# Kernel optimization log

Measured on AMD Instinct MI355X. Metric: run time of the kernel, lower is better.

## Reference

```python
import jax, jax.numpy as jnp
import numpy as np

B, N, T, D = 8, 32, 49, 4
K = 4            # edge_types
HE = 256         # encoder_hidden
HD = 256         # decoder_hidden (msg_hid == msg_out == n_hid)
TEMP = 0.5
SKIP_FIRST = True
EPS = 1e-5
E = N * (N - 1)  # 992 directed edges (off-diagonal)


def setup_inputs() -> dict:
    key = jax.random.key(0)
    ks = jax.random.split(key, 32)
    it = iter(range(32))

    def lin(fi, fo):
        k = ks[next(it)]
        return (jax.random.normal(k, (fi, fo), jnp.float32) / np.sqrt(fi)).astype(jnp.float32)

    def bias(fo):
        return jnp.full((fo,), 0.1, jnp.float32)

    off = ~np.eye(N, dtype=bool)
    recv_np, send_np = np.where(off)  # rel_rec rows, rel_send cols
    recv_idx = jnp.asarray(recv_np, jnp.int32)
    send_idx = jnp.asarray(send_np, jnp.int32)

    data = jax.random.normal(ks[next(it)], (B, N, T, D), jnp.float32)
    u = jax.random.uniform(ks[next(it)], (B, E, K), jnp.float32, 1e-6, 1.0 - 1e-6)
    gumbel = -jnp.log(-jnp.log(u))

    inp = {"data": data, "gumbel": gumbel, "recv_idx": recv_idx, "send_idx": send_idx}
    # Encoder: 4 MLPs (fc1, fc2, bn gamma/beta) + fc_out
    enc_dims = [(T * D, HE), (2 * HE, HE), (HE, HE), (3 * HE, HE)]
    for i, (fi, fh) in enumerate(enc_dims, start=1):
        inp[f"e{i}_w1"] = lin(fi, HE)
        inp[f"e{i}_b1"] = bias(HE)
        inp[f"e{i}_w2"] = lin(HE, HE)
        inp[f"e{i}_b2"] = bias(HE)
        inp[f"e{i}_g"] = jnp.ones((HE,), jnp.float32)
        inp[f"e{i}_be"] = jnp.zeros((HE,), jnp.float32)
    inp["fc_w"] = lin(HE, K)
    inp["fc_b"] = bias(K)
    # Decoder: per-edge-type message MLPs (stacked) + output MLP
    inp["mw1"] = jnp.stack([lin(2 * D, HD) for _ in range(K)])
    inp["mb1"] = jnp.zeros((K, HD), jnp.float32)
    inp["mw2"] = jnp.stack([lin(HD, HD) for _ in range(K)])
    inp["mb2"] = jnp.zeros((K, HD), jnp.float32)
    inp["ow1"] = lin(D + HD, HD)
    inp["ob1"] = jnp.zeros((HD,), jnp.float32)
    inp["ow2"] = lin(HD, HD)
    inp["ob2"] = jnp.zeros((HD,), jnp.float32)
    inp["ow3"] = lin(HD, D)
    inp["ob3"] = jnp.zeros((D,), jnp.float32)
    return inp


def _mlp(x, w1, b1, w2, b2, g, be):
    # Two-layer ELU net + batch norm over all leading dims (training-mode stats).
    x = jax.nn.elu(x @ w1 + b1)
    x = jax.nn.elu(x @ w2 + b2)
    m = x.mean(axis=(0, 1), keepdims=True)
    v = x.var(axis=(0, 1), keepdims=True)
    return (x - m) / jnp.sqrt(v + EPS) * g + be


def reference(data, gumbel, recv_idx, send_idx,
              e1_w1, e1_b1, e1_w2, e1_b2, e1_g, e1_be,
              e2_w1, e2_b1, e2_w2, e2_b2, e2_g, e2_be,
              e3_w1, e3_b1, e3_w2, e3_b2, e3_g, e3_be,
              e4_w1, e4_b1, e4_w2, e4_b2, e4_g, e4_be,
              fc_w, fc_b, mw1, mb1, mw2, mb2,
              ow1, ob1, ow2, ob2, ow3, ob3):
    # ---------- Encoder ----------
    x = data.reshape(B, N, T * D)
    x = _mlp(x, e1_w1, e1_b1, e1_w2, e1_b2, e1_g, e1_be)          # [B,N,HE]
    edges = jnp.concatenate([x[:, send_idx], x[:, recv_idx]], -1)  # [B,E,2HE]
    x = _mlp(edges, e2_w1, e2_b1, e2_w2, e2_b2, e2_g, e2_be)       # [B,E,HE]
    x_skip = x
    # edge2node: rel_rec^T @ x == scatter-add by receiver, then /N
    incoming = jnp.zeros((B, N, HE), x.dtype).at[:, recv_idx, :].add(x) / N
    x = _mlp(incoming, e3_w1, e3_b1, e3_w2, e3_b2, e3_g, e3_be)    # [B,N,HE]
    edges2 = jnp.concatenate([x[:, send_idx], x[:, recv_idx]], -1)  # [B,E,2HE]
    x = jnp.concatenate([edges2, x_skip], -1)                       # [B,E,3HE]
    x = _mlp(x, e4_w1, e4_b1, e4_w2, e4_b2, e4_g, e4_be)
    logits = x @ fc_w + fc_b                                        # [B,E,K]

    rel_type = jax.nn.softmax((logits + gumbel) / TEMP, axis=-1)    # gumbel-softmax (soft)
    prob = jax.nn.softmax(logits, axis=-1)

    # ---------- Decoder (pred_steps=1) ----------
    inputs = jnp.transpose(data, (0, 2, 1, 3))                      # [B,T,N,D]
    rt = rel_type[:, None, :, :]                                    # [B,1,E,K] broadcast over T
    senders = inputs[:, :, send_idx, :]                             # [B,T,E,D]
    receivers = inputs[:, :, recv_idx, :]
    pre_msg = jnp.concatenate([senders, receivers], -1)             # [B,T,E,2D]

    start = 1 if SKIP_FIRST else 0
    all_msgs = jnp.zeros((B, T, E, HD), pre_msg.dtype)
    for k in range(start, K):
        msg = jax.nn.relu(pre_msg @ mw1[k] + mb1[k])
        msg = jax.nn.relu(msg @ mw2[k] + mb2[k])
        all_msgs = all_msgs + msg * rt[..., k:k + 1]

    # scatter-sum messages to receiving nodes
    agg = jnp.zeros((B, T, N, HD), all_msgs.dtype).at[:, :, recv_idx, :].add(all_msgs)
    aug = jnp.concatenate([inputs, agg], -1)                        # [B,T,N,D+HD]
    p = jax.nn.relu(aug @ ow1 + ob1)
    p = jax.nn.relu(p @ ow2 + ob2)
    p = p @ ow3 + ob3
    step = inputs + p                                               # [B,T,N,D]

    output = jnp.transpose(step[:, :T - 1], (0, 2, 1, 3))           # [B,N,T-1,D]
    return (output, prob)
```

## Files before the change

kernel.cpp:

```cpp
#include <hip/hip_runtime.h>
#include <hip/hip_bf16.h>

#define NNODES 32
#define TSTEPS 49
#define NEDGE  992
#define ROWS_E 7936
#define ROWS_OUT 12544
#define EPSV 1e-5f

typedef __hip_bfloat16 bf16;
typedef __attribute__((ext_vector_type(8))) short bf16x8;
typedef __attribute__((ext_vector_type(4))) float f32x4;

__device__ inline float eluf(float x){ return x > 0.f ? x : (__expf(x) - 1.f); }
__device__ inline float bfu2f(unsigned short u){ unsigned v = ((unsigned)u) << 16; return *reinterpret_cast<float*>(&v); }
__device__ inline unsigned pack_bf16(float a, float b){
  __hip_bfloat16 ha = __float2bfloat16(a), hb = __float2bfloat16(b);
  unsigned short ua = *reinterpret_cast<unsigned short*>(&ha);
  unsigned short ub = *reinterpret_cast<unsigned short*>(&hb);
  return (unsigned)ua | ((unsigned)ub << 16);
}

__global__ void prep_weights(const float* e2w1, const float* e2w2, const float* e4w1, const float* e4w2,
                             const float* mw2, const float* ow1, const float* ow2,
                             const float* e2b1, const float* e4b1,
                             bf16* w2abT, bf16* w2bT, bf16* w4abT, bf16* w4cT, bf16* w4bT,
                             bf16* mw2T, bf16* ow1T, bf16* ow2T,
                             float* bias2, float* bias4, float* zerob){
  int i = blockIdx.x*256 + threadIdx.x;
  if (i < 131072){ int n=i>>8, c=i&255;
    w2abT[i] = __float2bfloat16(n<256 ? e2w1[c*256+n] : e2w1[(256+c)*256 + (n-256)]); return;} i-=131072;
  if (i < 65536){ int n=i>>8,c=i&255; w2bT[i]=__float2bfloat16(e2w2[c*256+n]); return;} i-=65536;
  if (i < 131072){ int n=i>>8,c=i&255;
    w4abT[i]=__float2bfloat16(n<256 ? e4w1[c*256+n] : e4w1[(256+c)*256+(n-256)]); return;} i-=131072;
  if (i < 65536){ int n=i>>8,c=i&255; w4cT[i]=__float2bfloat16(e4w1[(512+c)*256+n]); return;} i-=65536;
  if (i < 65536){ int n=i>>8,c=i&255; w4bT[i]=__float2bfloat16(e4w2[c*256+n]); return;} i-=65536;
  if (i < 262144){ int k=i>>16, r=i&65535; int n=r>>8,c=r&255;
    mw2T[i]=__float2bfloat16(mw2[(k*256+c)*256+n]); return;} i-=262144;
  if (i < 73728){ int n=i/288, c=i%288;
    ow1T[i]= (c<260)?__float2bfloat16(ow1[c*256+n]):__float2bfloat16(0.f); return;} i-=73728;
  if (i < 65536){ int n=i>>8,c=i&255; ow2T[i]=__float2bfloat16(ow2[c*256+n]); return;} i-=65536;
  if (i < 512){ bias2[i] = (i<256)?e2b1[i]:0.f; return;} i-=512;
  if (i < 512){ bias4[i] = (i<256)?e4b1[i]:0.f; return;} i-=512;
  if (i < 256){ zerob[i]=0.f; return; }
}

template<int KIN>
__global__ void small_mlp(const float* __restrict__ X, const float* __restrict__ w1, const float* __restrict__ b1,
                          const float* __restrict__ w2, const float* __restrict__ b2, float* __restrict__ H){
  __shared__ float xs[KIN];
  __shared__ float h1[256];
  int r = blockIdx.x, f = threadIdx.x;
  for (int c = f; c < KIN; c += 256) xs[c] = X[(size_t)r*KIN + c];
  __syncthreads();
  float acc = b1[f];
  for (int c = 0; c < KIN; c++) acc = fmaf(xs[c], w1[c*256+f], acc);
  h1[f] = eluf(acc);
  __syncthreads();
  float a2 = b2[f];
  for (int c = 0; c < 256; c++) a2 = fmaf(h1[c], w2[c*256+f], a2);
  H[(size_t)r*256 + f] = eluf(a2);
}

__global__ void bn_small(const float* __restrict__ H, const float* __restrict__ g, const float* __restrict__ be,
                         bf16* __restrict__ Xout){
  int f = threadIdx.x;
  float s = 0.f, s2 = 0.f;
  for (int r = 0; r < 256; r++){ float v = H[r*256+f]; s += v; s2 += v*v; }
  float m = s * (1.f/256.f), var = s2 * (1.f/256.f) - m*m;
  float sc = g[f] * rsqrtf(var + EPSV), sh = be[f] - m*sc;
  for (int r = 0; r < 256; r++) Xout[r*256+f] = __float2bfloat16(H[r*256+f]*sc + sh);
}

template<int K, int NCOLS, int ACT, bool OBF, int MT, bool STATS>
__global__ __launch_bounds__(256,4) void gemm_mfma(const bf16* __restrict__ A, const bf16* __restrict__ WT,
                                                   const float* __restrict__ bias, void* __restrict__ Y,
                                                   float* __restrict__ part){
  constexpr int NTW = NCOLS/64;
  int mb = blockIdx.x;
  int tid = threadIdx.x;
  int w = tid >> 6, l = tid & 63, l15 = l & 15, lq = l >> 4;
  f32x4 acc[MT/16][NTW];
  #pragma unroll
  for (int m = 0; m < MT/16; m++)
    #pragma unroll
    for (int nt = 0; nt < NTW; nt++) acc[m][nt] = (f32x4){0.f,0.f,0.f,0.f};
  const bf16* Ab = A + (size_t)mb*MT*K;
  int nw = w*(NCOLS/4);
  for (int s = 0; s < K/32; s++){
    int c0 = s*32 + lq*8;
    bf16x8 bfr[NTW];
    #pragma unroll
    for (int nt = 0; nt < NTW; nt++){
      int fcol = nw + nt*16 + l15;
      bfr[nt] = *reinterpret_cast<const bf16x8*>(WT + (size_t)fcol*K + c0);
    }
    #pragma unroll
    for (int m = 0; m < MT/16; m++){
      bf16x8 afr = *reinterpret_cast<const bf16x8*>(Ab + (size_t)(m*16 + l15)*K + c0);
      #pragma unroll
      for (int nt = 0; nt < NTW; nt++)
        acc[m][nt] = __builtin_amdgcn_mfma_f32_16x16x32_bf16(afr, bfr[nt], acc[m][nt], 0, 0, 0);
    }
  }
  #pragma unroll
  for (int nt = 0; nt < NTW; nt++){
    int fcol = nw + nt*16 + l15;
    float bv = bias[fcol];
    float cs = 0.f, cs2 = 0.f;
    #pragma unroll
    for (int m = 0; m < MT/16; m++){
      #pragma unroll
      for (int v = 0; v < 4; v++){
        int row = mb*MT + m*16 + lq*4 + v;
        float val = acc[m][nt][v] + bv;
        if (ACT == 1) val = fmaxf(val, 0.f);
        else if (ACT == 2) val = eluf(val);
        if (OBF) ((bf16*)Y)[(size_t)row*NCOLS + fcol] = __float2bfloat16(val);
        else     ((float*)Y)[(size_t)row*NCOLS + fcol] = val;
        if (STATS){ cs += val; cs2 += val*val; }
      }
    }
    if (STATS){
      cs  += __shfl_xor(cs, 16);  cs  += __shfl_xor(cs, 32);
      cs2 += __shfl_xor(cs2, 16); cs2 += __shfl_xor(cs2, 32);
      if (l < 16){ part[(size_t)mb*512 + fcol] = cs; part[(size_t)mb*512 + 256 + fcol] = cs2; }
    }
  }
}

__global__ void combine2(const bf16* __restrict__ SR, bf16* __restrict__ Y){
  int i = blockIdx.x*256 + threadIdx.x;
  int row = i >> 5, c8 = (i & 31)*8;
  int b = row / NEDGE, e = row % NEDGE;
  int rc = e / 31, jj = e % 31;
  int sn = jj + (jj >= rc);
  bf16x8 s8 = *reinterpret_cast<const bf16x8*>(SR + (size_t)(b*NNODES + sn)*512 + c8);
  bf16x8 r8 = *reinterpret_cast<const bf16x8*>(SR + (size_t)(b*NNODES + rc)*512 + 256 + c8);
  bf16x8 o;
  #pragma unroll
  for (int k = 0; k < 8; k++){
    float v = bfu2f((unsigned short)s8[k]) + bfu2f((unsigned short)r8[k]);
    v = eluf(v);
    __hip_bfloat16 h = __float2bfloat16(v);
    o[k] = *reinterpret_cast<short*>(&h);
  }
  *reinterpret_cast<bf16x8*>(Y + (size_t)row*256 + c8) = o;
}

__global__ void combine4(const bf16* __restrict__ SR, const float* __restrict__ Z, bf16* __restrict__ Y){
  int i = blockIdx.x*256 + threadIdx.x;
  int row = i >> 5, c8 = (i & 31)*8;
  int b = row / NEDGE, e = row % NEDGE;
  int rc = e / 31, jj = e % 31;
  int sn = jj + (jj >= rc);
  bf16x8 s8 = *reinterpret_cast<const bf16x8*>(SR + (size_t)(b*NNODES + sn)*512 + c8);
  bf16x8 r8 = *reinterpret_cast<const bf16x8*>(SR + (size_t)(b*NNODES + rc)*512 + 256 + c8);
  const float* zp = Z + (size_t)row*256 + c8;
  float4 z0 = *reinterpret_cast<const float4*>(zp);
  float4 z1 = *reinterpret_cast<const float4*>(zp+4);
  float zz[8] = {z0.x,z0.y,z0.z,z0.w,z1.x,z1.y,z1.z,z1.w};
  bf16x8 o;
  #pragma unroll
  for (int k = 0; k < 8; k++){
    float v = bfu2f((unsigned short)s8[k]) + bfu2f((unsigned short)r8[k]) + zz[k];
    v = eluf(v);
    __hip_bfloat16 h = __float2bfloat16(v);
    o[k] = *reinterpret_cast<short*>(&h);
  }
  *reinterpret_cast<bf16x8*>(Y + (size_t)row*256 + c8) = o;
}

__global__ void bn_finalize(const float* __restrict__ part, int nb, const float* __restrict__ g,
                            const float* __restrict__ be, float* __restrict__ prm, float nrows){
  int f = threadIdx.x;
  float s = 0.f, s2 = 0.f;
  for (int i = 0; i < nb; i++){ s += part[(size_t)i*512+f]; s2 += part[(size_t)i*512+256+f]; }
  float m = s / nrows, var = s2 / nrows - m*m;
  float sc = g[f] * rsqrtf(var + EPSV);
  prm[f] = sc; prm[256+f] = be[f] - m*sc;
}
__global__ void bn_apply(const float* __restrict__ Y, const float* __restrict__ prm, bf16* __restrict__ X){
  int i = blockIdx.x*256 + threadIdx.x;
  int c8 = (i & 31)*8;
  const float* yp = Y + (size_t)i*8;
  float4 a0 = *reinterpret_cast<const float4*>(yp);
  float4 a1 = *reinterpret_cast<const float4*>(yp+4);
  float4 s0 = *reinterpret_cast<const float4*>(prm + c8);
  float4 s1 = *reinterpret_cast<const float4*>(prm + c8 + 4);
  float4 h0 = *reinterpret_cast<const float4*>(prm + 256 + c8);
  float4 h1 = *reinterpret_cast<const float4*>(prm + 256 + c8 + 4);
  float vals[8] = {a0.x*s0.x+h0.x, a0.y*s0.y+h0.y, a0.z*s0.z+h0.z, a0.w*s0.w+h0.w,
                   a1.x*s1.x+h1.x, a1.y*s1.y+h1.y, a1.z*s1.z+h1.z, a1.w*s1.w+h1.w};
  bf16x8 o;
  #pragma unroll
  for (int k = 0; k < 8; k++){
    __hip_bfloat16 h = __float2bfloat16(vals[k]);
    o[k] = *reinterpret_cast<short*>(&h);
  }
  *reinterpret_cast<bf16x8*>(X + (size_t)i*8) = o;
}

__global__ void seg_incoming(const bf16* __restrict__ X2, float* __restrict__ inc){
  int bn = blockIdx.x; int b = bn >> 5, n = bn & 31;
  int f = threadIdx.x;
  const bf16* p = X2 + (size_t)(b*NEDGE + n*31)*256 + f;
  float s = 0.f;
  for (int j = 0; j < 31; j++) s += __bfloat162float(p[j*256]);
  inc[bn*256 + f] = s * (1.f/32.f);
}

__global__ void fc_softmax(const bf16* __restrict__ X4, const float* __restrict__ fcw, const float* __restrict__ fcb,
                           const float* __restrict__ gumbel, float* __restrict__ prob_out, float* __restrict__ rt){
  int r = blockIdx.x*256 + threadIdx.x;
  if (r >= ROWS_E) return;
  float l0 = fcb[0], l1 = fcb[1], l2 = fcb[2], l3 = fcb[3];
  const bf16* xr = X4 + (size_t)r*256;
  for (int c = 0; c < 256; c += 8){
    uint4 u = *reinterpret_cast<const uint4*>(xr + c);
    unsigned uu[4] = {u.x, u.y, u.z, u.w};
    #pragma unroll
    for (int q = 0; q < 4; q++){
      float x0 = bfu2f((unsigned short)(uu[q] & 0xffff));
      float x1 = bfu2f((unsigned short)(uu[q] >> 16));
      int cc = c + 2*q;
      float4 w0 = *reinterpret_cast<const float4*>(fcw + cc*4);
      float4 w1 = *reinterpret_cast<const float4*>(fcw + (cc+1)*4);
      l0 += x0*w0.x + x1*w1.x; l1 += x0*w0.y + x1*w1.y;
      l2 += x0*w0.z + x1*w1.z; l3 += x0*w0.w + x1*w1.w;
    }
  }
  float mx = fmaxf(fmaxf(l0,l1), fmaxf(l2,l3));
  float e0 = __expf(l0-mx), e1 = __expf(l1-mx), e2 = __expf(l2-mx), e3 = __expf(l3-mx);
  float inv = 1.f / (e0+e1+e2+e3);
  prob_out[(size_t)r*4+0] = e0*inv; prob_out[(size_t)r*4+1] = e1*inv;
  prob_out[(size_t)r*4+2] = e2*inv; prob_out[(size_t)r*4+3] = e3*inv;
  float4 gv = *reinterpret_cast<const float4*>(gumbel + (size_t)r*4);
  float t0 = (l0+gv.x)*2.f, t1 = (l1+gv.y)*2.f, t2 = (l2+gv.z)*2.f, t3 = (l3+gv.w)*2.f;
  float mx2 = fmaxf(fmaxf(t0,t1), fmaxf(t2,t3));
  float f0 = __expf(t0-mx2), f1 = __expf(t1-mx2), f2 = __expf(t2-mx2), f3 = __expf(t3-mx2);
  float inv2 = 1.f / (f0+f1+f2+f3);
  rt[(size_t)r*4+0] = f0*inv2; rt[(size_t)r*4+1] = f1*inv2;
  rt[(size_t)r*4+2] = f2*inv2; rt[(size_t)r*4+3] = f3*inv2;
}

__global__ __launch_bounds__(256,2) void decoder_msg(
    const float* __restrict__ data, const float* __restrict__ rt,
    const float* __restrict__ mw1, const float* __restrict__ mb1,
    const bf16* __restrict__ mw2T, const float* __restrict__ mb2,
    bf16* __restrict__ Aaug){
  __shared__ __align__(16) short hA[128*256];
  __shared__ __align__(16) float xn[32][4];
  __shared__ __align__(16) float rts_s[128][4];
  __shared__ __align__(16) float aggl[4][256];
  int bx = blockIdx.x;
  int bt = bx >> 3, rg = bx & 7;
  int b = bt / TSTEPS, t = bt % TSTEPS;
  int n0 = rg * 4;
  int tid = threadIdx.x;
  int w = tid >> 6, l = tid & 63, l15 = l & 15, lq = l >> 4;

  if (tid < 32){
    xn[tid][0] = data[((size_t)(b*NNODES + tid)*TSTEPS + t)*4 + 0];
    xn[tid][1] = data[((size_t)(b*NNODES + tid)*TSTEPS + t)*4 + 1];
    xn[tid][2] = data[((size_t)(b*NNODES + tid)*TSTEPS + t)*4 + 2];
    xn[tid][3] = data[((size_t)(b*NNODES + tid)*TSTEPS + t)*4 + 3];
  } else if (tid >= 64 && tid < 192){
    int r = tid - 64;
    int n = n0 + (r >> 5), j = r & 31;
    float4 rv = make_float4(0.f,0.f,0.f,0.f);
    if (j < 31) rv = *reinterpret_cast<const float4*>(rt + ((size_t)(b*NEDGE + n*31 + j))*4);
    *reinterpret_cast<float4*>(&rts_s[r][0]) = rv;
  }
  for (int i = tid; i < 1024; i += 256) ((float*)aggl)[i] = 0.f;
  __syncthreads();

  int p = tid & 127, hf = tid >> 7;
  int rc0 = n0 + 2*hf, rc1 = rc0 + 1;
  int c0b = 4*p;

  for (int kk = 1; kk < 4; kk++){
    {
      float wS0x,wS0y,wS1x,wS1y,wS2x,wS2y,wS3x,wS3y;
      float wR0x,wR0y,wR1x,wR1y,wR2x,wR2y,wR3x,wR3y;
      {
        float2 a0 = *reinterpret_cast<const float2*>(mw1 + (size_t)(kk*8+0)*256 + 2*p);
        float2 a1 = *reinterpret_cast<const float2*>(mw1 + (size_t)(kk*8+1)*256 + 2*p);
        float2 a2 = *reinterpret_cast<const float2*>(mw1 + (size_t)(kk*8+2)*256 + 2*p);
        float2 a3 = *reinterpret_cast<const float2*>(mw1 + (size_t)(kk*8+3)*256 + 2*p);
        float2 a4 = *reinterpret_cast<const float2*>(mw1 + (size_t)(kk*8+4)*256 + 2*p);
        float2 a5 = *reinterpret_cast<const float2*>(mw1 + (size_t)(kk*8+5)*256 + 2*p);
        float2 a6 = *reinterpret_cast<const float2*>(mw1 + (size_t)(kk*8+6)*256 + 2*p);
        float2 a7 = *reinterpret_cast<const float2*>(mw1 + (size_t)(kk*8+7)*256 + 2*p);
        wS0x=a0.x; wS0y=a0.y; wS1x=a1.x; wS1y=a1.y; wS2x=a2.x; wS2y=a2.y; wS3x=a3.x; wS3y=a3.y;
        wR0x=a4.x; wR0y=a4.y; wR1x=a5.x; wR1y=a5.y; wR2x=a6.x; wR2y=a6.y; wR3x=a7.x; wR3y=a7.y;
      }
      float2 bb = *reinterpret_cast<const float2*>(mb1 + kk*256 + 2*p);
      float Sa[32], Sb[32];
      #pragma unroll
      for (int nd = 0; nd < 32; nd++){
        float4 x = *reinterpret_cast<float4*>(&xn[nd][0]);
        Sa[nd] = fmaf(x.x,wS0x, fmaf(x.y,wS1x, fmaf(x.z,wS2x, fmaf(x.w,wS3x, bb.x))));
        Sb[nd] = fmaf(x.x,wS0y, fmaf(x.y,wS1y, fmaf(x.z,wS2y, fmaf(x.w,wS3y, bb.y))));
      }
      float4 x0 = *reinterpret_cast<float4*>(&xn[rc0][0]);
      float4 x1 = *reinterpret_cast<float4*>(&xn[rc1][0]);
      float Ra0 = fmaf(x0.x,wR0x, fmaf(x0.y,wR1x, fmaf(x0.z,wR2x, x0.w*wR3x)));
      float Rb0 = fmaf(x0.x,wR0y, fmaf(x0.y,wR1y, fmaf(x0.z,wR2y, x0.w*wR3y)));
      float Ra1 = fmaf(x1.x,wR0x, fmaf(x1.y,wR1x, fmaf(x1.z,wR2x, x1.w*wR3x)));
      float Rb1 = fmaf(x1.x,wR0y, fmaf(x1.y,wR1y, fmaf(x1.z,wR2y, x1.w*wR3y)));
      char* hAb = reinterpret_cast<char*>(hA);
      #pragma unroll
      for (int jj = 0; jj < 32; jj++){
        {
          int r = hf*64 + jj;
          unsigned pk = 0u;
          if (jj < 31){
            bool sel = (jj >= rc0);
            float sa = sel ? Sa[jj+1] : Sa[jj];
            float sb = sel ? Sb[jj+1] : Sb[jj];
            pk = pack_bf16(fmaxf(sa + Ra0, 0.f), fmaxf(sb + Rb0, 0.f));
          }
          *reinterpret_cast<unsigned*>(hAb + r*512 + (c0b ^ ((r & 7) << 4))) = pk;
        }
        {
          int r = hf*64 + 32 + jj;
          unsigned pk = 0u;
          if (jj < 31){
            bool sel = (jj >= rc1);
            float sa = sel ? Sa[jj+1] : Sa[jj];
            float sb = sel ? Sb[jj+1] : Sb[jj];
            pk = pack_bf16(fmaxf(sa + Ra1, 0.f), fmaxf(sb + Rb1, 0.f));
          }
          *reinterpret_cast<unsigned*>(hAb + r*512 + (c0b ^ ((r & 7) << 4))) = pk;
        }
      }
    }
    __syncthreads();

    f32x4 acc[8][4];
    #pragma unroll
    for (int m = 0; m < 8; m++)
      #pragma unroll
      for (int nt = 0; nt < 4; nt++) acc[m][nt] = (f32x4){0.f,0.f,0.f,0.f};
    const bf16* wk = mw2T + (size_t)kk*65536;
    for (int s = 0; s < 8; s++){
      int c0 = s*32 + lq*8;
      bf16x8 bfr[4];
      #pragma unroll
      for (int nt = 0; nt < 4; nt++){
        int fcol = w*64 + nt*16 + l15;
        bfr[nt] = *reinterpret_cast<const bf16x8*>(wk + (size_t)fcol*256 + c0);
      }
      #pragma unroll
      for (int m = 0; m < 8; m++){
        int rowm = m*16 + l15;
        int byteoff = rowm*512 + ((s*64 + lq*16) ^ ((rowm & 7) << 4));
        bf16x8 af = *reinterpret_cast<const bf16x8*>(reinterpret_cast<const char*>(hA) + byteoff);
        #pragma unroll
        for (int nt = 0; nt < 4; nt++)
          acc[m][nt] = __builtin_amdgcn_mfma_f32_16x16x32_bf16(af, bfr[nt], acc[m][nt], 0, 0, 0);
      }
    }
    #pragma unroll
    for (int m = 0; m < 8; m++){
      int g = m >> 1;
      #pragma unroll
      for (int nt = 0; nt < 4; nt++){
        int fcol = w*64 + nt*16 + l15;
        float bv = mb2[kk*256 + fcol];
        float ssum = 0.f;
        #pragma unroll
        for (int v = 0; v < 4; v++){
          int rowa = m*16 + lq*4 + v;
          float msg = fmaxf(acc[m][nt][v] + bv, 0.f);
          ssum += msg * rts_s[rowa][kk];
        }
        ssum += __shfl_xor(ssum, 16);
        ssum += __shfl_xor(ssum, 32);
        if (lq == 0) aggl[g][fcol] += ssum;
      }
    }
    __syncthreads();
  }

  for (int i = tid; i < 4*288; i += 256){
    int g = i / 288, c = i % 288;
    float val;
    if (c < 4)        val = xn[n0+g][c];
    else if (c < 260) val = aggl[g][c-4];
    else              val = 0.f;
    Aaug[(size_t)(bt*NNODES + n0 + g)*288 + c] = __float2bfloat16(val);
  }
}

__global__ void final_out(const bf16* __restrict__ P2, const float* __restrict__ ow3,
                          const float* __restrict__ ob3, const float* __restrict__ data,
                          float* __restrict__ out){
  int r = blockIdx.x*256 + threadIdx.x;
  if (r >= ROWS_OUT) return;
  int bt = r >> 5, n = r & 31;
  int b = bt / TSTEPS, t = bt % TSTEPS;
  float a0 = ob3[0], a1 = ob3[1], a2 = ob3[2], a3 = ob3[3];
  const bf16* pr = P2 + (size_t)r*256;
  for (int c = 0; c < 256; c += 8){
    uint4 u = *reinterpret_cast<const uint4*>(pr + c);
    unsigned uu[4] = {u.x, u.y, u.z, u.w};
    #pragma unroll
    for (int q = 0; q < 4; q++){
      float x0 = bfu2f((unsigned short)(uu[q] & 0xffff));
      float x1 = bfu2f((unsigned short)(uu[q] >> 16));
      int cc = c + 2*q;
      float4 w0 = *reinterpret_cast<const float4*>(ow3 + cc*4);
      float4 w1 = *reinterpret_cast<const float4*>(ow3 + (cc+1)*4);
      a0 += x0*w0.x + x1*w1.x; a1 += x0*w0.y + x1*w1.y;
      a2 += x0*w0.z + x1*w1.z; a3 += x0*w0.w + x1*w1.w;
    }
  }
  if (t < TSTEPS-1){
    float4 dv = *reinterpret_cast<const float4*>(data + ((size_t)(b*NNODES + n)*TSTEPS + t)*4);
    float4 o; o.x = dv.x + a0; o.y = dv.y + a1; o.z = dv.z + a2; o.w = dv.w + a3;
    *reinterpret_cast<float4*>(out + ((size_t)(b*NNODES + n)*(TSTEPS-1) + t)*4) = o;
  }
}

extern "C" void kernel_launch(void* const* d_in, const int* in_sizes, int n_in,
                              void* d_out, int out_size, void* d_ws, size_t ws_size,
                              hipStream_t stream){
  const float* data    = (const float*)d_in[0];
  const float* gumbel  = (const float*)d_in[1];
  const float* e1_w1=(const float*)d_in[4],  *e1_b1=(const float*)d_in[5],
             * e1_w2=(const float*)d_in[6],  *e1_b2=(const float*)d_in[7],
             * e1_g =(const float*)d_in[8],  *e1_be=(const float*)d_in[9];
  const float* e2_w1=(const float*)d_in[10], *e2_b1=(const float*)d_in[11],
             * e2_w2=(const float*)d_in[12], *e2_b2=(const float*)d_in[13],
             * e2_g =(const float*)d_in[14], *e2_be=(const float*)d_in[15];
  const float* e3_w1=(const float*)d_in[16], *e3_b1=(const float*)d_in[17],
             * e3_w2=(const float*)d_in[18], *e3_b2=(const float*)d_in[19],
             * e3_g =(const float*)d_in[20], *e3_be=(const float*)d_in[21];
  const float* e4_w1=(const float*)d_in[22], *e4_b1=(const float*)d_in[23],
             * e4_w2=(const float*)d_in[24], *e4_b2=(const float*)d_in[25],
             * e4_g =(const float*)d_in[26], *e4_be=(const float*)d_in[27];
  const float* fc_w=(const float*)d_in[28], *fc_b=(const float*)d_in[29];
  const float* mw1=(const float*)d_in[30], *mb1=(const float*)d_in[31];
  const float* mw2=(const float*)d_in[32], *mb2=(const float*)d_in[33];
  const float* ow1=(const float*)d_in[34], *ob1=(const float*)d_in[35];
  const float* ow2=(const float*)d_in[36], *ob2=(const float*)d_in[37];
  const float* ow3=(const float*)d_in[38], *ob3=(const float*)d_in[39];

  char* ws = (char*)d_ws;
  size_t off = 0;
  auto alloc = [&](size_t bytes)->void*{ void* p = ws + off; off = (off + bytes + 255) & ~(size_t)255; return p; };
  bf16* W2ABT= (bf16*)alloc((size_t)131072*2);
  bf16* W2BT = (bf16*)alloc((size_t)65536*2);
  bf16* W4ABT= (bf16*)alloc((size_t)131072*2);
  bf16* W4CT = (bf16*)alloc((size_t)65536*2);
  bf16* W4BT = (bf16*)alloc((size_t)65536*2);
  bf16* MW2T = (bf16*)alloc((size_t)262144*2);
  bf16* OW1T = (bf16*)alloc((size_t)73728*2);
  bf16* OW2T = (bf16*)alloc((size_t)65536*2);
  float* BIAS2=(float*)alloc((size_t)512*4);
  float* BIAS4=(float*)alloc((size_t)512*4);
  float* ZEROB=(float*)alloc((size_t)256*4);
  bf16* X1   = (bf16*)alloc((size_t)65536*2);
  float* HS  = (float*)alloc((size_t)65536*4);
  bf16* X3   = (bf16*)alloc((size_t)65536*2);
  bf16* SR2  = (bf16*)alloc((size_t)131072*2);
  bf16* SR4  = (bf16*)alloc((size_t)131072*2);
  float* Z4  = (float*)alloc((size_t)7936*256*4);
  bf16* YBF  = (bf16*)alloc((size_t)12544*256*2);
  float* YF32= (float*)alloc((size_t)7936*256*4);
  bf16* X2   = (bf16*)alloc((size_t)7936*256*2);
  bf16* X4   = (bf16*)alloc((size_t)7936*256*2);
  bf16* P2   = (bf16*)alloc((size_t)12544*256*2);
  float* INC = (float*)alloc((size_t)65536*4);
  float* RT  = (float*)alloc((size_t)7936*4*4);
  float* PART= (float*)alloc((size_t)248*512*4);
  float* PRM = (float*)alloc((size_t)512*4);
  bf16* AAUG = (bf16*)alloc((size_t)12544*288*2);

  float* out = (float*)d_out;
  float* prob_out = out + 49152;

  prep_weights<<<3365,256,0,stream>>>(e2_w1,e2_w2,e4_w1,e4_w2,mw2,ow1,ow2,e2_b1,e4_b1,
                                      W2ABT,W2BT,W4ABT,W4CT,W4BT,MW2T,OW1T,OW2T,BIAS2,BIAS4,ZEROB);
  small_mlp<196><<<256,256,0,stream>>>(data, e1_w1,e1_b1,e1_w2,e1_b2, HS);
  bn_small<<<1,256,0,stream>>>(HS, e1_g, e1_be, X1);
  gemm_mfma<256,512,0,true,32,false><<<8,256,0,stream>>>(X1, W2ABT, BIAS2, SR2, nullptr);
  combine2<<<992,256,0,stream>>>(SR2, YBF);
  gemm_mfma<256,256,2,false,32,true><<<248,256,0,stream>>>(YBF, W2BT, e2_b2, YF32, PART);
  bn_finalize<<<1,256,0,stream>>>(PART, 248, e2_g, e2_be, PRM, 7936.f);
  bn_apply<<<992,256,0,stream>>>(YF32, PRM, X2);
  seg_incoming<<<256,256,0,stream>>>(X2, INC);
  small_mlp<256><<<256,256,0,stream>>>(INC, e3_w1,e3_b1,e3_w2,e3_b2, HS);
  bn_small<<<1,256,0,stream>>>(HS, e3_g, e3_be, X3);
  gemm_mfma<256,512,0,true,32,false><<<8,256,0,stream>>>(X3, W4ABT, BIAS4, SR4, nullptr);
  gemm_mfma<256,256,0,false,32,false><<<248,256,0,stream>>>(X2, W4CT, ZEROB, Z4, nullptr);
  combine4<<<992,256,0,stream>>>(SR4, Z4, YBF);
  gemm_mfma<256,256,2,false,32,true><<<248,256,0,stream>>>(YBF, W4BT, e4_b2, YF32, PART);
  bn_finalize<<<1,256,0,stream>>>(PART, 248, e4_g, e4_be, PRM, 7936.f);
  bn_apply<<<992,256,0,stream>>>(YF32, PRM, X4);
  fc_softmax<<<31,256,0,stream>>>(X4, fc_w, fc_b, gumbel, prob_out, RT);
  decoder_msg<<<3136,256,0,stream>>>(data, RT, mw1, mb1, MW2T, mb2, AAUG);
  gemm_mfma<288,256,1,true,32,false><<<392,256,0,stream>>>(AAUG, OW1T, ob1, YBF, nullptr);
  gemm_mfma<256,256,1,true,32,false><<<392,256,0,stream>>>(YBF, OW2T, ob2, P2, nullptr);
  final_out<<<49,256,0,stream>>>(P2, ow3, ob3, data, out);
}
```

Before: 626.4 us.

## Halve decoder_msg tile to two receiver nodes per block for higher occupancy

```diff
diff --git a/kernel.cpp b/kernel.cpp
--- a/kernel.cpp
+++ b/kernel.cpp
@@ -14,11 +14,10 @@
 
 __device__ inline float eluf(float x){ return x > 0.f ? x : (__expf(x) - 1.f); }
 __device__ inline float bfu2f(unsigned short u){ unsigned v = ((unsigned)u) << 16; return *reinterpret_cast<float*>(&v); }
-__device__ inline unsigned pack_bf16(float a, float b){
-  __hip_bfloat16 ha = __float2bfloat16(a), hb = __float2bfloat16(b);
-  unsigned short ua = *reinterpret_cast<unsigned short*>(&ha);
-  unsigned short ub = *reinterpret_cast<unsigned short*>(&hb);
-  return (unsigned)ua | ((unsigned)ub << 16);
+__device__ inline unsigned cvt_pk_bf16(float lo, float hi){
+  unsigned r;
+  asm("v_cvt_pk_bf16_f32 %0, %1, %2" : "=v"(r) : "v"(lo), "v"(hi));
+  return r;
 }
 
 __global__ void prep_weights(const float* e2w1, const float* e2w2, const float* e4w1, const float* e4w2,
@@ -244,103 +243,97 @@
   rt[(size_t)r*4+2] = f2*inv2; rt[(size_t)r*4+3] = f3*inv2;
 }
 
-__global__ __launch_bounds__(256,2) void decoder_msg(
+__global__ __launch_bounds__(256,4) void decoder_msg(
     const float* __restrict__ data, const float* __restrict__ rt,
     const float* __restrict__ mw1, const float* __restrict__ mb1,
     const bf16* __restrict__ mw2T, const float* __restrict__ mb2,
     bf16* __restrict__ Aaug){
-  __shared__ __align__(16) short hA[128*256];
+  __shared__ __align__(16) short hA[64*256];
   __shared__ __align__(16) float xn[32][4];
-  __shared__ __align__(16) float rts_s[128][4];
-  __shared__ __align__(16) float aggl[4][256];
+  __shared__ __align__(16) float rts_s[64][4];
+  __shared__ __align__(16) float aggl[2][256];
   int bx = blockIdx.x;
-  int bt = bx >> 3, rg = bx & 7;
+  int bt = bx >> 4, rg = bx & 15;
   int b = bt / TSTEPS, t = bt % TSTEPS;
-  int n0 = rg * 4;
+  int n0 = rg * 2;
   int tid = threadIdx.x;
   int w = tid >> 6, l = tid & 63, l15 = l & 15, lq = l >> 4;
 
   if (tid < 32){
-    xn[tid][0] = data[((size_t)(b*NNODES + tid)*TSTEPS + t)*4 + 0];
-    xn[tid][1] = data[((size_t)(b*NNODES + tid)*TSTEPS + t)*4 + 1];
-    xn[tid][2] = data[((size_t)(b*NNODES + tid)*TSTEPS + t)*4 + 2];
-    xn[tid][3] = data[((size_t)(b*NNODES + tid)*TSTEPS + t)*4 + 3];
-  } else if (tid >= 64 && tid < 192){
+    *reinterpret_cast<float4*>(&xn[tid][0]) =
+        *reinterpret_cast<const float4*>(data + ((size_t)(b*NNODES + tid)*TSTEPS + t)*4);
+  } else if (tid >= 64 && tid < 128){
     int r = tid - 64;
     int n = n0 + (r >> 5), j = r & 31;
     float4 rv = make_float4(0.f,0.f,0.f,0.f);
     if (j < 31) rv = *reinterpret_cast<const float4*>(rt + ((size_t)(b*NEDGE + n*31 + j))*4);
     *reinterpret_cast<float4*>(&rts_s[r][0]) = rv;
   }
-  for (int i = tid; i < 1024; i += 256) ((float*)aggl)[i] = 0.f;
+  for (int i = tid; i < 512; i += 256) ((float*)aggl)[i] = 0.f;
+  {
+    unsigned* hw = reinterpret_cast<unsigned*>(hA);
+    hw[(tid < 128) ? (31*128 + tid) : (63*128 + (tid - 128))] = 0u;
+  }
   __syncthreads();
 
-  int p = tid & 127, hf = tid >> 7;
-  int rc0 = n0 + 2*hf, rc1 = rc0 + 1;
-  int c0b = 4*p;
+  int c2 = tid & 127;
+  int rh = tid >> 7;
+  int xorbase = 4*c2;
 
   for (int kk = 1; kk < 4; kk++){
     {
-      float wS0x,wS0y,wS1x,wS1y,wS2x,wS2y,wS3x,wS3y;
-      float wR0x,wR0y,wR1x,wR1y,wR2x,wR2y,wR3x,wR3y;
-      {
-        float2 a0 = *reinterpret_cast<const float2*>(mw1 + (size_t)(kk*8+0)*256 + 2*p);
-        float2 a1 = *reinterpret_cast<const float2*>(mw1 + (size_t)(kk*8+1)*256 + 2*p);
-        float2 a2 = *reinterpret_cast<const float2*>(mw1 + (size_t)(kk*8+2)*256 + 2*p);
-        float2 a3 = *reinterpret_cast<const float2*>(mw1 + (size_t)(kk*8+3)*256 + 2*p);
-        float2 a4 = *reinterpret_cast<const float2*>(mw1 + (size_t)(kk*8+4)*256 + 2*p);
-        float2 a5 = *reinterpret_cast<const float2*>(mw1 + (size_t)(kk*8+5)*256 + 2*p);
-        float2 a6 = *reinterpret_cast<const float2*>(mw1 + (size_t)(kk*8+6)*256 + 2*p);
-        float2 a7 = *reinterpret_cast<const float2*>(mw1 + (size_t)(kk*8+7)*256 + 2*p);
-        wS0x=a0.x; wS0y=a0.y; wS1x=a1.x; wS1y=a1.y; wS2x=a2.x; wS2y=a2.y; wS3x=a3.x; wS3y=a3.y;
-        wR0x=a4.x; wR0y=a4.y; wR1x=a5.x; wR1y=a5.y; wR2x=a6.x; wR2y=a6.y; wR3x=a7.x; wR3y=a7.y;
+      float2 a0 = *reinterpret_cast<const float2*>(mw1 + (size_t)(kk*8+0)*256 + 2*c2);
+      float2 a1 = *reinterpret_cast<const float2*>(mw1 + (size_t)(kk*8+1)*256 + 2*c2);
+      float2 a2 = *reinterpret_cast<const float2*>(mw1 + (size_t)(kk*8+2)*256 + 2*c2);
+      float2 a3 = *reinterpret_cast<const float2*>(mw1 + (size_t)(kk*8+3)*256 + 2*c2);
+      float2 a4 = *reinterpret_cast<const float2*>(mw1 + (size_t)(kk*8+4)*256 + 2*c2);
+      float2 a5 = *reinterpret_cast<const float2*>(mw1 + (size_t)(kk*8+5)*256 + 2*c2);
+      float2 a6 = *reinterpret_cast<const float2*>(mw1 + (size_t)(kk*8+6)*256 + 2*c2);
+      float2 a7 = *reinterpret_cast<const float2*>(mw1 + (size_t)(kk*8+7)*256 + 2*c2);
+      float2 bb = *reinterpret_cast<const float2*>(mb1 + kk*256 + 2*c2);
+      float Sa[17], Sb[17];
+      #pragma unroll
+      for (int i = 0; i < 17; i++){
+        int nd = rh*16 + i; if (nd > 31) nd = 31;
+        float4 x = *reinterpret_cast<float4*>(&xn[nd][0]);
+        Sa[i] = fmaf(x.x,a0.x, fmaf(x.y,a1.x, fmaf(x.z,a2.x, fmaf(x.w,a3.x, bb.x))));
+        Sb[i] = fmaf(x.x,a0.y, fmaf(x.y,a1.y, fmaf(x.z,a2.y, fmaf(x.w,a3.y, bb.y))));
       }
-      float2 bb = *reinterpret_cast<const float2*>(mb1 + kk*256 + 2*p);
-      float Sa[32], Sb[32];
-      #pragma unroll
-      for (int nd = 0; nd < 32; nd++){
-        float4 x = *reinterpret_cast<float4*>(&xn[nd][0]);
-        Sa[nd] = fmaf(x.x,wS0x, fmaf(x.y,wS1x, fmaf(x.z,wS2x, fmaf(x.w,wS3x, bb.x))));
-        Sb[nd] = fmaf(x.x,wS0y, fmaf(x.y,wS1y, fmaf(x.z,wS2y, fmaf(x.w,wS3y, bb.y))));
-      }
-      float4 x0 = *reinterpret_cast<float4*>(&xn[rc0][0]);
-      float4 x1 = *reinterpret_cast<float4*>(&xn[rc1][0]);
-      float Ra0 = fmaf(x0.x,wR0x, fmaf(x0.y,wR1x, fmaf(x0.z,wR2x, x0.w*wR3x)));
-      float Rb0 = fmaf(x0.x,wR0y, fmaf(x0.y,wR1y, fmaf(x0.z,wR2y, x0.w*wR3y)));
-      float Ra1 = fmaf(x1.x,wR0x, fmaf(x1.y,wR1x, fmaf(x1.z,wR2x, x1.w*wR3x)));
-      float Rb1 = fmaf(x1.x,wR0y, fmaf(x1.y,wR1y, fmaf(x1.z,wR2y, x1.w*wR3y)));
+      float4 x0 = *reinterpret_cast<float4*>(&xn[n0][0]);
+      float4 x1 = *reinterpret_cast<float4*>(&xn[n0+1][0]);
+      float Ra0 = fmaf(x0.x,a4.x, fmaf(x0.y,a5.x, fmaf(x0.z,a6.x, x0.w*a7.x)));
+      float Rb0 = fmaf(x0.x,a4.y, fmaf(x0.y,a5.y, fmaf(x0.z,a6.y, x0.w*a7.y)));
+      float Ra1 = fmaf(x1.x,a4.x, fmaf(x1.y,a5.x, fmaf(x1.z,a6.x, x1.w*a7.x)));
+      float Rb1 = fmaf(x1.x,a4.y, fmaf(x1.y,a5.y, fmaf(x1.z,a6.y, x1.w*a7.y)));
       char* hAb = reinterpret_cast<char*>(hA);
       #pragma unroll
-      for (int jj = 0; jj < 32; jj++){
-        {
-          int r = hf*64 + jj;
-          unsigned pk = 0u;
-          if (jj < 31){
-            bool sel = (jj >= rc0);
-            float sa = sel ? Sa[jj+1] : Sa[jj];
-            float sb = sel ? Sb[jj+1] : Sb[jj];
-            pk = pack_bf16(fmaxf(sa + Ra0, 0.f), fmaxf(sb + Rb0, 0.f));
+      for (int ii = 0; ii < 16; ii++){
+        int aj = rh*16 + ii;
+        if (aj < 31){
+          {
+            bool sel = (aj >= n0);
+            float sa = sel ? Sa[ii+1] : Sa[ii];
+            float sb = sel ? Sb[ii+1] : Sb[ii];
+            unsigned pk = cvt_pk_bf16(fmaxf(sa + Ra0, 0.f), fmaxf(sb + Rb0, 0.f));
+            int r = aj;
+            *reinterpret_cast<unsigned*>(hAb + r*512 + (xorbase ^ ((r & 7) << 4))) = pk;
           }
-          *reinterpret_cast<unsigned*>(hAb + r*512 + (c0b ^ ((r & 7) << 4))) = pk;
-        }
-        {
-          int r = hf*64 + 32 + jj;
-          unsigned pk = 0u;
-          if (jj < 31){
-            bool sel = (jj >= rc1);
-            float sa = sel ? Sa[jj+1] : Sa[jj];
-            float sb = sel ? Sb[jj+1] : Sb[jj];
-            pk = pack_bf16(fmaxf(sa + Ra1, 0.f), fmaxf(sb + Rb1, 0.f));
+          {
+            bool sel = (aj >= n0+1);
+            float sa = sel ? Sa[ii+1] : Sa[ii];
+            float sb = sel ? Sb[ii+1] : Sb[ii];
+            unsigned pk = cvt_pk_bf16(fmaxf(sa + Ra1, 0.f), fmaxf(sb + Rb1, 0.f));
+            int r = 32 + aj;
+            *reinterpret_cast<unsigned*>(hAb + r*512 + (xorbase ^ ((r & 7) << 4))) = pk;
           }
-          *reinterpret_cast<unsigned*>(hAb + r*512 + (c0b ^ ((r & 7) << 4))) = pk;
         }
       }
     }
     __syncthreads();
 
-    f32x4 acc[8][4];
-    #pragma unroll
-    for (int m = 0; m < 8; m++)
+    f32x4 acc[4][4];
+    #pragma unroll
+    for (int m = 0; m < 4; m++)
       #pragma unroll
       for (int nt = 0; nt < 4; nt++) acc[m][nt] = (f32x4){0.f,0.f,0.f,0.f};
     const bf16* wk = mw2T + (size_t)kk*65536;
@@ -353,7 +346,7 @@
         bfr[nt] = *reinterpret_cast<const bf16x8*>(wk + (size_t)fcol*256 + c0);
       }
       #pragma unroll
-      for (int m = 0; m < 8; m++){
+      for (int m = 0; m < 4; m++){
         int rowm = m*16 + l15;
         int byteoff = rowm*512 + ((s*64 + lq*16) ^ ((rowm & 7) << 4));
         bf16x8 af = *reinterpret_cast<const bf16x8*>(reinterpret_cast<const char*>(hA) + byteoff);
@@ -363,7 +356,7 @@
       }
     }
     #pragma unroll
-    for (int m = 0; m < 8; m++){
+    for (int m = 0; m < 4; m++){
       int g = m >> 1;
       #pragma unroll
       for (int nt = 0; nt < 4; nt++){
@@ -384,7 +377,7 @@
     __syncthreads();
   }
 
-  for (int i = tid; i < 4*288; i += 256){
+  for (int i = tid; i < 2*288; i += 256){
     int g = i / 288, c = i % 288;
     float val;
     if (c < 4)        val = xn[n0+g][c];
@@ -501,7 +494,7 @@
   bn_finalize<<<1,256,0,stream>>>(PART, 248, e4_g, e4_be, PRM, 7936.f);
   bn_apply<<<992,256,0,stream>>>(YF32, PRM, X4);
   fc_softmax<<<31,256,0,stream>>>(X4, fc_w, fc_b, gumbel, prob_out, RT);
-  decoder_msg<<<3136,256,0,stream>>>(data, RT, mw1, mb1, MW2T, mb2, AAUG);
+  decoder_msg<<<6272,256,0,stream>>>(data, RT, mw1, mb1, MW2T, mb2, AAUG);
   gemm_mfma<288,256,1,true,32,false><<<392,256,0,stream>>>(AAUG, OW1T, ob1, YBF, nullptr);
   gemm_mfma<256,256,1,true,32,false><<<392,256,0,stream>>>(YBF, OW2T, ob2, P2, nullptr);
   final_out<<<49,256,0,stream>>>(P2, ow3, ob3, data, out);
```

Result: slower. 840.0 us (+34.1%).
